# Performance work log

Measured on AMD Instinct MI355X. Metric: run time of the kernel, lower is better.

Reference implementation:

```python
import jax, jax.numpy as jnp
import numpy as np

N = 50000      # nodes
E = 800000     # edges (avg degree 16)
D = 64         # hidden_dim = heads * per-head channels
H = 4          # heads
C = D // H     # per-head channels
EDIM = 16      # edge feature dim
L = 3          # num_layers
NEG_SLOPE = 0.2


def setup_inputs() -> dict:
    key = jax.random.key(0)
    ks = jax.random.split(key, 11)
    s = 0.1
    return {
        "x": jax.random.normal(ks[0], (N, D), dtype=jnp.float32),
        "edge_index": jax.random.randint(ks[1], (2, E), 0, N, dtype=jnp.int32),
        "edge_attr": jax.random.normal(ks[2], (E, EDIM), dtype=jnp.float32),
        # stacked per-layer GATv2 parameters (all layers have in=out=D)
        "Wl": jax.random.normal(ks[3], (L, D, D), dtype=jnp.float32) * s,
        "bl": jnp.zeros((L, D), dtype=jnp.float32),
        "Wr": jax.random.normal(ks[4], (L, D, D), dtype=jnp.float32) * s,
        "br": jnp.zeros((L, D), dtype=jnp.float32),
        "We": jax.random.normal(ks[5], (L, EDIM, D), dtype=jnp.float32) * s,
        "att": jax.random.normal(ks[6], (L, H, C), dtype=jnp.float32) * s,
        "bias": jnp.zeros((L, D), dtype=jnp.float32),
    }


def _gatv2_layer(x, src, dst, edge_attr, Wl, bl, Wr, br, We, att, bias):
    # x: [N, D] -> out: [N, D] (concat of H heads of C channels)
    xl = (x @ Wl + bl).reshape(N, H, C)          # source transform (message value)
    xr = (x @ Wr + br).reshape(N, H, C)          # target transform
    ef = (edge_attr @ We).reshape(E, H, C)       # edge feature transform
    m = jax.nn.leaky_relu(xl[src] + xr[dst] + ef, NEG_SLOPE)  # [E, H, C]
    score = jnp.einsum('ehc,hc->eh', m, att)     # [E, H]
    # segment softmax over incoming edges of each target node
    smax = jax.ops.segment_max(score, dst, num_segments=N)   # [N, H]
    ex = jnp.exp(score - smax[dst])                          # [E, H]
    denom = jax.ops.segment_sum(ex, dst, num_segments=N)     # [N, H]
    alpha = ex / denom[dst]                                  # [E, H]
    out = jax.ops.segment_sum(alpha[:, :, None] * xl[src], dst, num_segments=N)
    return out.reshape(N, D) + bias


def reference(x, edge_index, edge_attr, Wl, bl, Wr, br, We, att, bias):
    src, dst = edge_index[0], edge_index[1]
    h = x
    for l in range(L):
        h = _gatv2_layer(h, src, dst, edge_attr,
                         Wl[l], bl[l], Wr[l], br[l], We[l], att[l], bias[l])
        h = jax.nn.relu(h)
    return h
```

## Files before the change

kernel.cpp:

```cpp
#include <hip/hip_runtime.h>
#include <cfloat>

#define NEG_SLOPE 0.2f

__global__ __launch_bounds__(256) void zero_kernel(int* __restrict__ counts,
                                                   int* __restrict__ cursor, int n) {
    int gid = blockIdx.x * 256 + threadIdx.x;
    if (gid < n) { counts[gid] = 0; cursor[gid] = 0; }
}

__global__ __launch_bounds__(256) void count_kernel(const int* __restrict__ dst,
                                                    int* __restrict__ counts, int E) {
    int e = blockIdx.x * 256 + threadIdx.x;
    if (e < E) atomicAdd(&counts[dst[e]], 1);
}

__global__ __launch_bounds__(256) void scan_bsums_kernel(const int* __restrict__ counts,
                                                         int* __restrict__ bsums, int N) {
    int t = threadIdx.x;
    int base = blockIdx.x * 1024 + t * 4;
    int s = 0;
    #pragma unroll
    for (int i = 0; i < 4; ++i) { int idx = base + i; if (idx < N) s += counts[idx]; }
    #pragma unroll
    for (int d = 1; d < 64; d <<= 1) s += __shfl_xor(s, d);
    __shared__ int ws[4];
    if ((t & 63) == 0) ws[t >> 6] = s;
    __syncthreads();
    if (t == 0) bsums[blockIdx.x] = ws[0] + ws[1] + ws[2] + ws[3];
}

__global__ __launch_bounds__(64) void scan_bscan_kernel(int* __restrict__ bsums, int NB) {
    int t = threadIdx.x;
    int v = (t < NB) ? bsums[t] : 0;
    int x = v;
    #pragma unroll
    for (int d = 1; d < 64; d <<= 1) {
        int y = __shfl_up(x, d);
        if (t >= d) x += y;
    }
    if (t < NB) bsums[t] = x - v;
}

__global__ __launch_bounds__(256) void scan_final_kernel(const int* __restrict__ counts,
                                                         const int* __restrict__ bsums,
                                                         int* __restrict__ offs, int N) {
    int t = threadIdx.x, lane = t & 63, w = t >> 6;
    int base = blockIdx.x * 1024 + t * 4;
    int v[4]; int s = 0;
    #pragma unroll
    for (int i = 0; i < 4; ++i) { int idx = base + i; v[i] = (idx < N) ? counts[idx] : 0; s += v[i]; }
    int x = s;
    #pragma unroll
    for (int d = 1; d < 64; d <<= 1) {
        int y = __shfl_up(x, d);
        if (lane >= d) x += y;
    }
    __shared__ int wtot[4];
    if (lane == 63) wtot[w] = x;
    __syncthreads();
    int wexc = 0;
    for (int i = 0; i < w; ++i) wexc += wtot[i];
    int run = (x - s) + wexc + bsums[blockIdx.x];
    #pragma unroll
    for (int i = 0; i < 4; ++i) {
        int idx = base + i;
        run += v[i];
        if (idx < N) offs[idx + 1] = run;
    }
    if (blockIdx.x == 0 && t == 0) offs[0] = 0;
}

__global__ __launch_bounds__(256) void scatter_kernel(
    const int* __restrict__ src, const int* __restrict__ dst,
    const int* __restrict__ offs, int* __restrict__ cursor,
    int4* __restrict__ csr, int E) {
    int e = blockIdx.x * 256 + threadIdx.x;
    if (e >= E) return;
    int d = dst[e];
    int pos = offs[d] + atomicAdd(&cursor[d], 1);
    csr[pos] = make_int4(src[e], d, e, 0);
}

__global__ __launch_bounds__(256) void sort_segments_kernel(
    int4* __restrict__ csr, const int* __restrict__ offs, int N)
{
    int t = threadIdx.x;
    int lane = t & 63;
    int node = blockIdx.x * 4 + (t >> 6);
    if (node >= N) return;
    int off = offs[node];
    int deg = offs[node + 1] - off;
    if (deg <= 1) return;
    if (deg <= 64) {
        int key = 0x7FFFFFFF; int4 kv = make_int4(0, 0, 0, 0);
        if (lane < deg) { kv = csr[off + lane]; key = kv.z; }
        int rank = 0;
        #pragma unroll
        for (int i = 0; i < 64; ++i) {
            int ki = __shfl(key, i);
            if (ki < key) rank++;
        }
        if (lane < deg) csr[off + rank] = kv;
    } else if (lane == 0) {
        for (int a = 1; a < deg; ++a) {
            int4 kv = csr[off + a];
            int b = a - 1;
            while (b >= 0 && csr[off + b].z > kv.z) {
                csr[off + b + 1] = csr[off + b];
                b--;
            }
            csr[off + b + 1] = kv;
        }
    }
}

__global__ __launch_bounds__(256) void eaperm_kernel(
    const float* __restrict__ ea, const int4* __restrict__ csr,
    float* __restrict__ eaperm, int E)
{
    int gid = blockIdx.x * 256 + threadIdx.x;
    int pos = gid >> 2, q = gid & 3;
    if (pos >= E) return;
    int eid = csr[pos].z;
    *(float4*)(eaperm + (size_t)pos * 16 + q * 4) =
        *(const float4*)(ea + (size_t)eid * 16 + q * 4);
}

#define XSTRIDE 68
__global__ __launch_bounds__(256) void node_gemm_kernel(
    const float* __restrict__ hin,
    const float* __restrict__ Wl, const float* __restrict__ bl,
    const float* __restrict__ Wr, const float* __restrict__ br,
    float* __restrict__ xl, float* __restrict__ xr, int nrows)
{
    __shared__ float sWl[4096];
    __shared__ float sWr[4096];
    __shared__ float sX[64 * XSTRIDE];
    int t = threadIdx.x;
    {
        float4* dl = (float4*)sWl; const float4* sl = (const float4*)Wl;
        float4* dr = (float4*)sWr; const float4* sr = (const float4*)Wr;
        for (int i = t; i < 1024; i += 256) { dl[i] = sl[i]; dr[i] = sr[i]; }
    }
    int row0 = blockIdx.x * 64;
    for (int i = t; i < 1024; i += 256) {
        int rr = i >> 4;
        int cc = (i & 15) << 2;
        int row = row0 + rr;
        float4 v = make_float4(0.f, 0.f, 0.f, 0.f);
        if (row < nrows) v = *(const float4*)(hin + (size_t)row * 64 + cc);
        *(float4*)(&sX[rr * XSTRIDE + cc]) = v;
    }
    __syncthreads();

    int lane = t & 63;
    int w = t >> 6;
    int rs = lane >> 4;
    int c4 = lane & 15;
    float4 bl4 = *(const float4*)(bl + c4 * 4);
    float4 br4 = *(const float4*)(br + c4 * 4);

    #pragma unroll
    for (int g = 0; g < 4; ++g) {
        int rloc = w * 16 + g * 4 + rs;
        int row = row0 + rloc;
        float4 al = {0.f, 0.f, 0.f, 0.f};
        float4 ar = {0.f, 0.f, 0.f, 0.f};
        const float* xrow = &sX[rloc * XSTRIDE];
        #pragma unroll 4
        for (int k = 0; k < 64; ++k) {
            float xk = xrow[k];
            float4 wl4 = *(const float4*)(&sWl[k * 64 + c4 * 4]);
            float4 wr4 = *(const float4*)(&sWr[k * 64 + c4 * 4]);
            al.x += xk * wl4.x; al.y += xk * wl4.y;
            al.z += xk * wl4.z; al.w += xk * wl4.w;
            ar.x += xk * wr4.x; ar.y += xk * wr4.y;
            ar.z += xk * wr4.z; ar.w += xk * wr4.w;
        }
        if (row < nrows) {
            float4 ol, orr;
            ol.x = al.x + bl4.x; ol.y = al.y + bl4.y;
            ol.z = al.z + bl4.z; ol.w = al.w + bl4.w;
            orr.x = ar.x + br4.x; orr.y = ar.y + br4.y;
            orr.z = ar.z + br4.z; orr.w = ar.w + br4.w;
            *(float4*)(xl + (size_t)row * 64 + c4 * 4) = ol;
            *(float4*)(xr + (size_t)row * 64 + c4 * 4) = orr;
        }
    }
}

__global__ __launch_bounds__(256) void edge_score_kernel(
    const float* __restrict__ xl, const float* __restrict__ xr,
    const float* __restrict__ ea, const float* __restrict__ eaperm, int use_perm,
    const int4* __restrict__ csr,
    const float* __restrict__ We, const float* __restrict__ att,
    float* __restrict__ score_csr, int E)
{
    __shared__ float sWe[1024];
    __shared__ float sAtt[64];
    int t = threadIdx.x;
    for (int i = t; i < 1024; i += 256) sWe[i] = We[i];
    if (t < 64) sAtt[t] = att[t];
    __syncthreads();
    int gid = blockIdx.x * 256 + t;
    int pos = gid >> 2, h = gid & 3;
    if (pos >= E) return;
    int4 se = csr[pos];
    int s = se.x, d = se.y;
    const float4* eap = use_perm
        ? (const float4*)(eaperm + (size_t)pos * 16)
        : (const float4*)(ea + (size_t)se.z * 16);
    float4 a0 = eap[0], a1 = eap[1], a2 = eap[2], a3 = eap[3];
    float av[16] = {a0.x, a0.y, a0.z, a0.w, a1.x, a1.y, a1.z, a1.w,
                    a2.x, a2.y, a2.z, a2.w, a3.x, a3.y, a3.z, a3.w};
    const float4* xls = (const float4*)(xl + (size_t)s * 64 + h * 16);
    const float4* xrd = (const float4*)(xr + (size_t)d * 64 + h * 16);
    float4 vl0 = xls[0], vl1 = xls[1], vl2 = xls[2], vl3 = xls[3];
    float4 vr0 = xrd[0], vr1 = xrd[1], vr2 = xrd[2], vr3 = xrd[3];

    float ef[16];
    #pragma unroll
    for (int c = 0; c < 16; ++c) ef[c] = 0.f;
    #pragma unroll
    for (int k = 0; k < 16; ++k) {
        float a = av[k];
        const float* wrow = &sWe[k * 64 + h * 16];
        #pragma unroll
        for (int c = 0; c < 16; ++c) ef[c] += a * wrow[c];
    }

    float lv[16] = {vl0.x, vl0.y, vl0.z, vl0.w, vl1.x, vl1.y, vl1.z, vl1.w,
                    vl2.x, vl2.y, vl2.z, vl2.w, vl3.x, vl3.y, vl3.z, vl3.w};
    float rv[16] = {vr0.x, vr0.y, vr0.z, vr0.w, vr1.x, vr1.y, vr1.z, vr1.w,
                    vr2.x, vr2.y, vr2.z, vr2.w, vr3.x, vr3.y, vr3.z, vr3.w};
    float sc0 = 0.f, sc1 = 0.f, sc2 = 0.f, sc3 = 0.f;
    #pragma unroll
    for (int c = 0; c < 16; c += 4) {
        float m0 = lv[c] + rv[c] + ef[c];
        float m1 = lv[c+1] + rv[c+1] + ef[c+1];
        float m2 = lv[c+2] + rv[c+2] + ef[c+2];
        float m3 = lv[c+3] + rv[c+3] + ef[c+3];
        m0 = (m0 >= 0.f) ? m0 : NEG_SLOPE * m0;
        m1 = (m1 >= 0.f) ? m1 : NEG_SLOPE * m1;
        m2 = (m2 >= 0.f) ? m2 : NEG_SLOPE * m2;
        m3 = (m3 >= 0.f) ? m3 : NEG_SLOPE * m3;
        sc0 += m0 * sAtt[h * 16 + c];
        sc1 += m1 * sAtt[h * 16 + c + 1];
        sc2 += m2 * sAtt[h * 16 + c + 2];
        sc3 += m3 * sAtt[h * 16 + c + 3];
    }
    score_csr[gid] = (sc0 + sc1) + (sc2 + sc3);
}

__global__ __launch_bounds__(256) void node_pass_kernel(
    const float* __restrict__ score_csr, const float* __restrict__ xl,
    const int4* __restrict__ csr,
    const int* __restrict__ offs, const float* __restrict__ bias,
    float* __restrict__ hout, int N)
{
    int t = threadIdx.x;
    int lane = t & 63;
    int node = blockIdx.x * 4 + (t >> 6);
    if (node >= N) return;
    int eg = lane >> 4;
    int k  = lane & 15;
    int h  = k >> 2;
    int off = offs[node];
    int deg = offs[node + 1] - off;

    if (deg == 0) {
        if (eg == 0) {
            float4 b = *(const float4*)(bias + k * 4);
            float4 o;
            o.x = fmaxf(b.x, 0.f); o.y = fmaxf(b.y, 0.f);
            o.z = fmaxf(b.z, 0.f); o.w = fmaxf(b.w, 0.f);
            *(float4*)(hout + (size_t)node * 64 + k * 4) = o;
        }
        return;
    }

    float mx = -FLT_MAX;
    for (int j0 = 0; j0 < deg; j0 += 4) {
        int j = j0 + eg;
        if (j < deg) {
            float sc = score_csr[(size_t)(off + j) * 4 + h];
            mx = fmaxf(mx, sc);
        }
    }
    mx = fmaxf(mx, __shfl_xor(mx, 16));
    mx = fmaxf(mx, __shfl_xor(mx, 32));

    float4 acc = {0.f, 0.f, 0.f, 0.f};
    float sSum = 0.f;
    for (int j0 = 0; j0 < deg; j0 += 4) {
        int j = j0 + eg;
        int jj = (j < deg) ? j : deg - 1;
        int pos = off + jj;
        int s = csr[pos].x;
        float sc = score_csr[(size_t)pos * 4 + h];
        float ex = (j < deg) ? __expf(sc - mx) : 0.f;
        float4 v = *(const float4*)(xl + (size_t)s * 64 + k * 4);
        acc.x += ex * v.x; acc.y += ex * v.y;
        acc.z += ex * v.z; acc.w += ex * v.w;
        sSum += ex;
    }

    acc.x += __shfl_xor(acc.x, 16); acc.y += __shfl_xor(acc.y, 16);
    acc.z += __shfl_xor(acc.z, 16); acc.w += __shfl_xor(acc.w, 16);
    sSum  += __shfl_xor(sSum, 16);
    acc.x += __shfl_xor(acc.x, 32); acc.y += __shfl_xor(acc.y, 32);
    acc.z += __shfl_xor(acc.z, 32); acc.w += __shfl_xor(acc.w, 32);
    sSum  += __shfl_xor(sSum, 32);

    if (eg == 0) {
        float inv = 1.f / sSum;
        float4 b = *(const float4*)(bias + k * 4);
        float4 o;
        o.x = fmaxf(acc.x * inv + b.x, 0.f);
        o.y = fmaxf(acc.y * inv + b.y, 0.f);
        o.z = fmaxf(acc.z * inv + b.z, 0.f);
        o.w = fmaxf(acc.w * inv + b.w, 0.f);
        *(float4*)(hout + (size_t)node * 64 + k * 4) = o;
    }
}

extern "C" void kernel_launch(void* const* d_in, const int* in_sizes, int n_in,
                              void* d_out, int out_size, void* d_ws, size_t ws_size,
                              hipStream_t stream) {
    const float* x    = (const float*)d_in[0];
    const int*   eidx = (const int*)d_in[1];
    const float* ea   = (const float*)d_in[2];
    const float* Wl   = (const float*)d_in[3];
    const float* bl   = (const float*)d_in[4];
    const float* Wr   = (const float*)d_in[5];
    const float* br   = (const float*)d_in[6];
    const float* We   = (const float*)d_in[7];
    const float* att  = (const float*)d_in[8];
    const float* bias = (const float*)d_in[9];
    float* out = (float*)d_out;

    const int N = in_sizes[0] / 64;
    const int E = in_sizes[1] / 2;
    const int* src = eidx;
    const int* dst = eidx + E;

    float* ws = (float*)d_ws;
    float* xl      = ws;
    float* xr      = xl + (size_t)N * 64;
    float* score   = xr + (size_t)N * 64;
    float* h_tmp   = score + (size_t)E * 4;
    int* counts    = (int*)(h_tmp + (size_t)N * 64);
    int* cursor    = counts + N;
    int* offs      = cursor + N;
    int* bsums     = offs + N + 1;
    uintptr_t p    = (uintptr_t)(bsums + 64);
    p = (p + 15) & ~(uintptr_t)15;
    int4* csr      = (int4*)p;
    float* eaperm  = (float*)(csr + E);

    size_t need_base = (uintptr_t)(eaperm) - (uintptr_t)d_ws;
    size_t need_perm = need_base + (size_t)E * 16 * sizeof(float);
    int use_perm = (ws_size >= need_perm) ? 1 : 0;

    dim3 blk(256);
    int g_n    = (N + 255) / 256;
    int g_e    = (E + 255) / 256;
    int g_eh   = (E * 4 + 255) / 256;
    int g_gemm = (N + 63) / 64;
    int g_node = (N + 3) / 4;
    int NB     = (N + 1023) / 1024;

    zero_kernel<<<g_n, blk, 0, stream>>>(counts, cursor, N);
    count_kernel<<<g_e, blk, 0, stream>>>(dst, counts, E);
    scan_bsums_kernel<<<NB, blk, 0, stream>>>(counts, bsums, N);
    scan_bscan_kernel<<<1, 64, 0, stream>>>(bsums, NB);
    scan_final_kernel<<<NB, blk, 0, stream>>>(counts, bsums, offs, N);
    scatter_kernel<<<g_e, blk, 0, stream>>>(src, dst, offs, cursor, csr, E);
    sort_segments_kernel<<<g_node, blk, 0, stream>>>(csr, offs, N);
    if (use_perm)
        eaperm_kernel<<<g_eh, blk, 0, stream>>>(ea, csr, eaperm, E);

    const float* hin = x;
    for (int l = 0; l < 3; ++l) {
        float* hout = (l == 2) ? out : h_tmp;
        node_gemm_kernel<<<g_gemm, blk, 0, stream>>>(hin, Wl + (size_t)l * 4096, bl + l * 64,
                                                     Wr + (size_t)l * 4096, br + l * 64, xl, xr, N);
        edge_score_kernel<<<g_eh, blk, 0, stream>>>(xl, xr, ea, eaperm, use_perm, csr,
                                                    We + (size_t)l * 1024, att + l * 64,
                                                    score, E);
        node_pass_kernel<<<g_node, blk, 0, stream>>>(score, xl, csr, offs,
                                                     bias + l * 64, hout, N);
        hin = hout;
    }
}
```

Baseline: 527.1 us.

## Drop permuted edge-attribute copy and batch four edges per scatter thread

Removes the eaperm kernel and its workspace buffer, so edge_score now gathers edge attributes directly through the CSR edge id in every layer. The aim is to save one full permute pass over the 16-float edge features. The cost is that the gather in each of the three layers becomes scattered instead of contiguous. The scatter kernel also now handles four edges per thread, which lets several loads and atomics be in flight at once.

```diff
diff --git a/kernel.cpp b/kernel.cpp
--- a/kernel.cpp
+++ b/kernel.cpp
@@ -75,11 +75,22 @@
     const int* __restrict__ src, const int* __restrict__ dst,
     const int* __restrict__ offs, int* __restrict__ cursor,
     int4* __restrict__ csr, int E) {
-    int e = blockIdx.x * 256 + threadIdx.x;
-    if (e >= E) return;
-    int d = dst[e];
-    int pos = offs[d] + atomicAdd(&cursor[d], 1);
-    csr[pos] = make_int4(src[e], d, e, 0);
+    int base = (blockIdx.x * 256 + threadIdx.x) * 4;
+    if (base >= E) return;
+    int n = E - base; if (n > 4) n = 4;
+    int s0[4], d0[4], p0[4];
+    #pragma unroll
+    for (int i = 0; i < 4; ++i) {
+        if (i < n) { s0[i] = src[base + i]; d0[i] = dst[base + i]; }
+    }
+    #pragma unroll
+    for (int i = 0; i < 4; ++i) {
+        if (i < n) p0[i] = offs[d0[i]] + atomicAdd(&cursor[d0[i]], 1);
+    }
+    #pragma unroll
+    for (int i = 0; i < 4; ++i) {
+        if (i < n) csr[p0[i]] = make_int4(s0[i], d0[i], base + i, 0);
+    }
 }
 
 __global__ __launch_bounds__(256) void sort_segments_kernel(
@@ -113,18 +124,6 @@
             csr[off + b + 1] = kv;
         }
     }
-}
-
-__global__ __launch_bounds__(256) void eaperm_kernel(
-    const float* __restrict__ ea, const int4* __restrict__ csr,
-    float* __restrict__ eaperm, int E)
-{
-    int gid = blockIdx.x * 256 + threadIdx.x;
-    int pos = gid >> 2, q = gid & 3;
-    if (pos >= E) return;
-    int eid = csr[pos].z;
-    *(float4*)(eaperm + (size_t)pos * 16 + q * 4) =
-        *(const float4*)(ea + (size_t)eid * 16 + q * 4);
 }
 
 #define XSTRIDE 68
@@ -192,7 +191,7 @@
 
 __global__ __launch_bounds__(256) void edge_score_kernel(
     const float* __restrict__ xl, const float* __restrict__ xr,
-    const float* __restrict__ ea, const float* __restrict__ eaperm, int use_perm,
+    const float* __restrict__ ea,
     const int4* __restrict__ csr,
     const float* __restrict__ We, const float* __restrict__ att,
     float* __restrict__ score_csr, int E)
@@ -208,9 +207,7 @@
     if (pos >= E) return;
     int4 se = csr[pos];
     int s = se.x, d = se.y;
-    const float4* eap = use_perm
-        ? (const float4*)(eaperm + (size_t)pos * 16)
-        : (const float4*)(ea + (size_t)se.z * 16);
+    const float4* eap = (const float4*)(ea + (size_t)se.z * 16);
     float4 a0 = eap[0], a1 = eap[1], a2 = eap[2], a3 = eap[3];
     float av[16] = {a0.x, a0.y, a0.z, a0.w, a1.x, a1.y, a1.z, a1.w,
                     a2.x, a2.y, a2.z, a2.w, a3.x, a3.y, a3.z, a3.w};
@@ -357,15 +354,11 @@
     uintptr_t p    = (uintptr_t)(bsums + 64);
     p = (p + 15) & ~(uintptr_t)15;
     int4* csr      = (int4*)p;
-    float* eaperm  = (float*)(csr + E);
-
-    size_t need_base = (uintptr_t)(eaperm) - (uintptr_t)d_ws;
-    size_t need_perm = need_base + (size_t)E * 16 * sizeof(float);
-    int use_perm = (ws_size >= need_perm) ? 1 : 0;
 
     dim3 blk(256);
     int g_n    = (N + 255) / 256;
     int g_e    = (E + 255) / 256;
+    int g_e4   = (E + 1023) / 1024;
     int g_eh   = (E * 4 + 255) / 256;
     int g_gemm = (N + 63) / 64;
     int g_node = (N + 3) / 4;
@@ -376,17 +369,15 @@
     scan_bsums_kernel<<<NB, blk, 0, stream>>>(counts, bsums, N);
     scan_bscan_kernel<<<1, 64, 0, stream>>>(bsums, NB);
     scan_final_kernel<<<NB, blk, 0, stream>>>(counts, bsums, offs, N);
-    scatter_kernel<<<g_e, blk, 0, stream>>>(src, dst, offs, cursor, csr, E);
+    scatter_kernel<<<g_e4, blk, 0, stream>>>(src, dst, offs, cursor, csr, E);
     sort_segments_kernel<<<g_node, blk, 0, stream>>>(csr, offs, N);
-    if (use_perm)
-        eaperm_kernel<<<g_eh, blk, 0, stream>>>(ea, csr, eaperm, E);
 
     const float* hin = x;
     for (int l = 0; l < 3; ++l) {
         float* hout = (l == 2) ? out : h_tmp;
         node_gemm_kernel<<<g_gemm, blk, 0, stream>>>(hin, Wl + (size_t)l * 4096, bl + l * 64,
                                                      Wr + (size_t)l * 4096, br + l * 64, xl, xr, N);
-        edge_score_kernel<<<g_eh, blk, 0, stream>>>(xl, xr, ea, eaperm, use_perm, csr,
+        edge_score_kernel<<<g_eh, blk, 0, stream>>>(xl, xr, ea, csr,
                                                     We + (size_t)l * 1024, att + l * 64,
                                                     score, E);
         node_pass_kernel<<<g_node, blk, 0, stream>>>(score, xl, csr, offs,
```

Result: no change. 518.9 us (-1.6%).
